# Optimization experiments

Measured on AMD Instinct MI355X. Metric: run time of the kernel, lower is better.

## Reference

```python
import jax, jax.numpy as jnp
import numpy as np

NUM_NODES = 100000
NUM_REL = 3
IN_C, HID_C, OUT_C = 128, 64, 32
E, P = 1600000, 200000


def setup_inputs() -> dict:
    key = jax.random.key(0)
    ks = jax.random.split(key, 16)
    inp = {
        "x": jax.random.normal(ks[0], (NUM_NODES, IN_C), dtype=jnp.float32),
        "edge_index": jax.random.randint(ks[1], (2, E), 0, NUM_NODES),
        "edge_type": jax.random.randint(ks[2], (E,), 0, NUM_REL),
        "pred_edges": jax.random.randint(ks[3], (2, P), 0, NUM_NODES),
        # RGCN layer 1
        "W1": jax.random.normal(ks[4], (NUM_REL, IN_C, HID_C), dtype=jnp.float32) * 0.05,
        "root1": jax.random.normal(ks[5], (IN_C, HID_C), dtype=jnp.float32) * 0.05,
        "b1": jnp.zeros((HID_C,), dtype=jnp.float32),
        # RGCN layer 2
        "W2": jax.random.normal(ks[6], (NUM_REL, HID_C, OUT_C), dtype=jnp.float32) * 0.05,
        "root2": jax.random.normal(ks[7], (HID_C, OUT_C), dtype=jnp.float32) * 0.05,
        "b2": jnp.zeros((OUT_C,), dtype=jnp.float32),
        # decoder MLP: Linear(2*OUT_C, HID_C) -> ReLU -> Linear(HID_C, 1)
        "Wd1": jax.random.normal(ks[8], (2 * OUT_C, HID_C), dtype=jnp.float32) * 0.05,
        "bd1": jnp.zeros((HID_C,), dtype=jnp.float32),
        "Wd2": jax.random.normal(ks[9], (HID_C, 1), dtype=jnp.float32) * 0.05,
        "bd2": jnp.zeros((1,), dtype=jnp.float32),
    }
    return inp


def rgcn_conv(x, edge_index, edge_type, W, root, b):
    """PyG RGCNConv: per-relation mean aggregation + root transform + bias."""
    src, dst = edge_index[0], edge_index[1]
    n = x.shape[0]
    xs = x[src]  # [E, in] single gather reused across relations
    out = x @ root + b
    for r in range(W.shape[0]):  # small fixed relation count
        mask = (edge_type == r)
        msg = jnp.where(mask[:, None], xs @ W[r], 0.0)  # [E, out]
        summed = jax.ops.segment_sum(msg, dst, num_segments=n)
        cnt = jax.ops.segment_sum(mask.astype(x.dtype), dst, num_segments=n)
        out = out + summed / jnp.maximum(cnt, 1.0)[:, None]
    return out


def reference(x, edge_index, edge_type, pred_edges, W1, root1, b1, W2, root2, b2, Wd1, bd1, Wd2, bd2):
    # encode (eval mode: dropout is identity)
    z = jax.nn.relu(rgcn_conv(x, edge_index, edge_type, W1, root1, b1))
    z = rgcn_conv(z, edge_index, edge_type, W2, root2, b2)
    # decode
    src, dst = pred_edges[0], pred_edges[1]
    ef = jnp.concatenate([z[src], z[dst]], axis=1)  # [P, 2*OUT_C]
    h = jax.nn.relu(ef @ Wd1 + bd1)
    return (h @ Wd2 + bd2).squeeze(-1)  # [P]
```

## Files before the change

### kernel.cpp

```cpp
#include <hip/hip_runtime.h>
#include <hip/hip_bf16.h>


typedef short bf16x8 __attribute__((ext_vector_type(8)));
typedef float f32x4 __attribute__((ext_vector_type(4)));
typedef float f32x2 __attribute__((ext_vector_type(2)));

__device__ __forceinline__ unsigned short f2bf(float f) {
  union { float f; unsigned u; } x; x.f = f;
  unsigned r = x.u + 0x7FFF + ((x.u >> 16) & 1);
  return (unsigned short)(r >> 16);
}
__device__ __forceinline__ float bf2f(unsigned short h) {
  union { unsigned u; float f; } x; x.u = ((unsigned)h) << 16;
  return x.f;
}
__device__ __forceinline__ f32x2 bfpair(unsigned u) {
  union { unsigned u; float f; } a, b;
  a.u = u << 16; b.u = u & 0xFFFF0000u;
  f32x2 r; r[0] = a.f; r[1] = b.f; return r;
}
__device__ __forceinline__ unsigned pk2(float a, float b) {
  return (unsigned)f2bf(a) | ((unsigned)f2bf(b) << 16);
}

template <int K, int TN>
__device__ __forceinline__ void pack_one(
    int e, const float* __restrict__ W, const float* __restrict__ root,
    ushort* __restrict__ Bh, ushort* __restrict__ Bl) {
  int slab = e / (K * TN), r = e % (K * TN);
  int k = r / TN, n = r % TN;
  float v = (slab < 3) ? W[(size_t)slab * K * TN + k * TN + n] : root[(size_t)k * TN + n];
  int kc = k >> 5, quad = (k >> 3) & 3, j = k & 7, nt = n >> 4, nn = n & 15;
  int NTt = TN / 16;
  int didx = slab * K * TN + ((kc * NTt + nt) * 64 + quad * 16 + nn) * 8 + j;
  unsigned short h = f2bf(v);
  Bh[didx] = h;
  Bl[didx] = f2bf(v - bf2f(h));
}

__global__ __launch_bounds__(256) void hist_pack_kernel(
    const int* __restrict__ ei, int* __restrict__ hist, int E, int tile, int NBUCK,
    const float* __restrict__ W1, const float* __restrict__ root1,
    ushort* __restrict__ Bh1, ushort* __restrict__ Bl1,
    const float* __restrict__ W2, const float* __restrict__ root2,
    ushort* __restrict__ Bh2, ushort* __restrict__ Bl2) {
  int tid = threadIdx.x;
  if (blockIdx.x >= 256) {
    int e = (blockIdx.x - 256) * 256 + tid;
    if (e < 32768) pack_one<128, 64>(e, W1, root1, Bh1, Bl1);
    else if (e < 32768 + 8192) pack_one<64, 32>(e - 32768, W2, root2, Bh2, Bl2);
    return;
  }
  __shared__ int lh[512];
  for (int i = tid; i < 512; i += 256) lh[i] = 0;
  __syncthreads();
  int e0 = blockIdx.x * tile, e1 = min(E, e0 + tile);
  for (int e = e0 + tid; e < e1; e += 256) atomicAdd(&lh[ei[E + e] >> 8], 1);
  __syncthreads();
  for (int i = tid; i < NBUCK; i += 256) hist[i * 256 + blockIdx.x] = lh[i];
}

__global__ __launch_bounds__(256) void scan_rows_kernel(
    int* __restrict__ hist, int* __restrict__ rowsum) {
  __shared__ int sA[256], sB[256];
  int t = threadIdx.x;
  int* row = hist + blockIdx.x * 256;
  int v = row[t];
  sA[t] = v;
  __syncthreads();
  int* src = sA; int* dst = sB;
  for (int off = 1; off < 256; off <<= 1) {
    int x = src[t];
    if (t >= off) x += src[t - off];
    dst[t] = x;
    __syncthreads();
    int* tmp = src; src = dst; dst = tmp;
  }
  row[t] = src[t] - v;
  if (t == 255) rowsum[blockIdx.x] = src[255];
}

__global__ __launch_bounds__(512) void scan_top_kernel(
    const int* __restrict__ rowsum, int* __restrict__ rowbase, int NBUCK, int E) {
  __shared__ int sA[512], sB[512];
  int t = threadIdx.x;
  int v = (t < NBUCK) ? rowsum[t] : 0;
  sA[t] = v;
  __syncthreads();
  int* src = sA; int* dst = sB;
  for (int off = 1; off < 512; off <<= 1) {
    int x = src[t];
    if (t >= off) x += src[t - off];
    dst[t] = x;
    __syncthreads();
    int* tmp = src; src = dst; dst = tmp;
  }
  if (t < NBUCK) rowbase[t] = src[t] - v;
  if (t == 0) rowbase[NBUCK] = E;
}

__global__ __launch_bounds__(256) void part_scatter_kernel(
    const int* __restrict__ ei, const int* __restrict__ et,
    const int* __restrict__ hist, const int* __restrict__ rowbase,
    unsigned* __restrict__ rec, int E, int tile, int NBUCK) {
  __shared__ int ctr[512];
  int tid = threadIdx.x;
  for (int i = tid; i < NBUCK; i += 256)
    ctr[i] = hist[i * 256 + blockIdx.x] + rowbase[i];
  __syncthreads();
  int e0 = blockIdx.x * tile, e1 = min(E, e0 + tile);
  for (int e = e0 + tid; e < e1; e += 256) {
    int s = ei[e];
    int d = ei[E + e];
    int t = et[e];
    int p = atomicAdd(&ctr[d >> 8], 1);
    rec[p] = (unsigned)(s | (t << 20) | ((d & 255) << 22));
  }
}

__global__ __launch_bounds__(256) void bucket_build_kernel(
    const unsigned* __restrict__ rec, const int* __restrict__ rowbase,
    float4* __restrict__ inv4, int2* __restrict__ sd,
    int* __restrict__ eSrcT, int N) {
  __shared__ int c3[768];
  __shared__ int sA[256], sB[256];
  __shared__ int cur[256];
  int tid = threadIdx.x;
  int dstBase = blockIdx.x << 8;
  int bs = rowbase[blockIdx.x], be = rowbase[blockIdx.x + 1];
  for (int i = tid; i < 768; i += 256) c3[i] = 0;
  __syncthreads();
  for (int i = bs + tid; i < be; i += 256) {
    unsigned r = rec[i];
    atomicAdd(&c3[((r >> 20) & 3) * 256 + (r >> 22)], 1);
  }
  __syncthreads();
  int c0 = c3[tid], c1 = c3[256 + tid], c2 = c3[512 + tid];
  int dgv = c0 + c1 + c2;
  sA[tid] = dgv;
  if (dstBase + tid < N) {
    inv4[dstBase + tid] = make_float4(1.0f / (float)max(c0, 1),
                                      1.0f / (float)max(c1, 1),
                                      1.0f / (float)max(c2, 1), 0.f);
  }
  __syncthreads();
  int* src = sA; int* dst = sB;
  for (int off = 1; off < 256; off <<= 1) {
    int x = src[tid];
    if (tid >= off) x += src[tid - off];
    dst[tid] = x;
    __syncthreads();
    int* tmp = src; src = dst; dst = tmp;
  }
  int excl = src[tid] - dgv;
  cur[tid] = bs + excl;
  if (dstBase + tid < N) sd[dstBase + tid] = make_int2(bs + excl, dgv);
  __syncthreads();
  for (int i = bs + tid; i < be; i += 256) {
    unsigned r = rec[i];
    int p = atomicAdd(&cur[r >> 22], 1);
    eSrcT[p] = (int)(r & 0x3FFFFF);
  }
}

template <int K, int TN>
__global__ __launch_bounds__(256, 4) void mfma_gemm_kernel(
    const float* __restrict__ A, const ushort* __restrict__ Bh,
    const ushort* __restrict__ Bl, const float* __restrict__ bias,
    ushort* __restrict__ Hb, float* __restrict__ z, int n) {
  constexpr int KC = K / 32;
  constexpr int NTt = TN / 16;
  constexpr int HALF = K * TN / 8;
  __shared__ int4 bsm[2 * HALF];
  const int tid = threadIdx.x;
  const int w = tid >> 6, lane = tid & 63;
  const int quad = lane >> 4, nn = lane & 15;
  const int rowBase = blockIdx.x * 64 + w * 16;

  int row = rowBase + nn;
  if (row >= n) row = n - 1;
  const float* ap = &A[(size_t)row * K + quad * 8];
  bf16x8 ah[KC], al[KC];
#pragma unroll
  for (int kc = 0; kc < KC; kc++) {
    float4 f0 = *(const float4*)(ap + kc * 32);
    float4 f1 = *(const float4*)(ap + kc * 32 + 4);
    float f[8] = {f0.x, f0.y, f0.z, f0.w, f1.x, f1.y, f1.z, f1.w};
#pragma unroll
    for (int j = 0; j < 8; j++) {
      unsigned short h = f2bf(f[j]);
      ah[kc][j] = (short)h;
      al[kc][j] = (short)f2bf(f[j] - bf2f(h));
    }
  }

  const short* bsp = (const short*)bsm;

#pragma unroll 1
  for (int slab = 0; slab < 4; slab++) {
    __syncthreads();
    {
      const int4* gh = (const int4*)(Bh + (size_t)slab * K * TN);
      for (int i = tid; i < HALF; i += 256) bsm[i] = gh[i];
      if (slab == 3) {
        const int4* gl = (const int4*)(Bl + (size_t)slab * K * TN);
        for (int i = tid; i < HALF; i += 256) bsm[HALF + i] = gl[i];
      }
    }
    __syncthreads();

    f32x4 acc[NTt];
#pragma unroll
    for (int j = 0; j < NTt; j++) acc[j] = (f32x4){0.f, 0.f, 0.f, 0.f};

#pragma unroll
    for (int kc = 0; kc < KC; kc++) {
#pragma unroll
      for (int nt = 0; nt < NTt; nt++) {
        bf16x8 b = *(const bf16x8*)&bsp[((kc * NTt + nt) * 64 + lane) * 8];
        acc[nt] = __builtin_amdgcn_mfma_f32_16x16x32_bf16(ah[kc], b, acc[nt], 0, 0, 0);
        acc[nt] = __builtin_amdgcn_mfma_f32_16x16x32_bf16(al[kc], b, acc[nt], 0, 0, 0);
      }
    }
    if (slab == 3) {
#pragma unroll
      for (int kc = 0; kc < KC; kc++) {
#pragma unroll
        for (int nt = 0; nt < NTt; nt++) {
          bf16x8 b = *(const bf16x8*)&bsp[(HALF * 8) + ((kc * NTt + nt) * 64 + lane) * 8];
          acc[nt] = __builtin_amdgcn_mfma_f32_16x16x32_bf16(ah[kc], b, acc[nt], 0, 0, 0);
        }
      }
    }

    int grow0 = rowBase + quad * 4;
#pragma unroll
    for (int nt = 0; nt < NTt; nt++) {
      int col = nt * 16 + nn;
#pragma unroll
      for (int rg = 0; rg < 4; rg++) {
        int grow = grow0 + rg;
        if (grow < n) {
          float v = acc[nt][rg];
          if (slab == 3) z[(size_t)grow * TN + col] = v + bias[col];
          else Hb[((size_t)slab * n + grow) * TN + col] = f2bf(v);
        }
      }
    }
  }
}

__global__ __launch_bounds__(256, 4) void mfma_gemm2_kernel(
    const ushort* __restrict__ Ab, const ushort* __restrict__ Bh,
    const ushort* __restrict__ Bl, const float* __restrict__ bias,
    ushort* __restrict__ Hb, float* __restrict__ z2r, int n) {
  constexpr int KC = 2, NTt = 2, HALF = 64 * 32 / 8;
  __shared__ int4 bsm[2 * HALF];
  const int tid = threadIdx.x;
  const int w = tid >> 6, lane = tid & 63;
  const int quad = lane >> 4, nn = lane & 15;
  const int rowBase = blockIdx.x * 64 + w * 16;

  int row = rowBase + nn;
  if (row >= n) row = n - 1;
  const ushort* ap = &Ab[(size_t)row * 64 + quad * 8];
  bf16x8 ah[KC];
  ah[0] = *(const bf16x8*)(ap);
  ah[1] = *(const bf16x8*)(ap + 32);

  const short* bsp = (const short*)bsm;

#pragma unroll 1
  for (int slab = 0; slab < 4; slab++) {
    __syncthreads();
    {
      const int4* gh = (const int4*)(Bh + (size_t)slab * 64 * 32);
      for (int i = tid; i < HALF; i += 256) bsm[i] = gh[i];
      if (slab == 3) {
        const int4* gl = (const int4*)(Bl + (size_t)slab * 64 * 32);
        for (int i = tid; i < HALF; i += 256) bsm[HALF + i] = gl[i];
      }
    }
    __syncthreads();

    f32x4 acc[NTt];
#pragma unroll
    for (int j = 0; j < NTt; j++) acc[j] = (f32x4){0.f, 0.f, 0.f, 0.f};

#pragma unroll
    for (int kc = 0; kc < KC; kc++) {
#pragma unroll
      for (int nt = 0; nt < NTt; nt++) {
        bf16x8 b = *(const bf16x8*)&bsp[((kc * NTt + nt) * 64 + lane) * 8];
        acc[nt] = __builtin_amdgcn_mfma_f32_16x16x32_bf16(ah[kc], b, acc[nt], 0, 0, 0);
      }
    }
    if (slab == 3) {
#pragma unroll
      for (int kc = 0; kc < KC; kc++) {
#pragma unroll
        for (int nt = 0; nt < NTt; nt++) {
          bf16x8 b = *(const bf16x8*)&bsp[(HALF * 8) + ((kc * NTt + nt) * 64 + lane) * 8];
          acc[nt] = __builtin_amdgcn_mfma_f32_16x16x32_bf16(ah[kc], b, acc[nt], 0, 0, 0);
        }
      }
    }

    int grow0 = rowBase + quad * 4;
#pragma unroll
    for (int nt = 0; nt < NTt; nt++) {
      int col = nt * 16 + nn;
#pragma unroll
      for (int rg = 0; rg < 4; rg++) {
        int grow = grow0 + rg;
        if (grow < n) {
          float v = acc[nt][rg];
          if (slab == 3) z2r[(size_t)grow * 32 + col] = v + bias[col];
          else Hb[((size_t)slab * n + grow) * 32 + col] = f2bf(v);
        }
      }
    }
  }
}

__global__ __launch_bounds__(256) void pull64_kernel(
    const ushort* __restrict__ Hb, const int* __restrict__ eSrcT,
    const int2* __restrict__ sd, const float4* __restrict__ inv4,
    const float* __restrict__ z1r, ushort* __restrict__ z1b, int N) {
  int w = (blockIdx.x * 256 + threadIdx.x) >> 6;
  if (w >= N) return;
  int lane = threadIdx.x & 63;
  int g = lane >> 3, q = lane & 7;
  int2 s2 = sd[w];
  float4 iv = inv4[w];
  f32x2 acc0 = {0.f, 0.f}, acc1 = acc0, acc2 = acc0, acc3 = acc0;
  for (int i = g; i < s2.y; i += 8) {
    int p = eSrcT[s2.x + i];
    int s = p & 0xFFFFF, t = p >> 20;
    float sc = (t == 0) ? iv.x : ((t == 1) ? iv.y : iv.z);
    f32x2 sc2 = {sc, sc};
    uint4 v = *(const uint4*)&Hb[((size_t)t * N + s) * 64 + q * 8];
    acc0 += bfpair(v.x) * sc2;
    acc1 += bfpair(v.y) * sc2;
    acc2 += bfpair(v.z) * sc2;
    acc3 += bfpair(v.w) * sc2;
  }
  float a[8] = {acc0[0], acc0[1], acc1[0], acc1[1], acc2[0], acc2[1], acc3[0], acc3[1]};
#pragma unroll
  for (int m = 8; m <= 32; m <<= 1)
#pragma unroll
    for (int j = 0; j < 8; j++) a[j] += __shfl_xor(a[j], m);
  if (g == 0) {
    const float4* zr = (const float4*)&z1r[(size_t)w * 64 + q * 8];
    float4 r0 = zr[0], r1 = zr[1];
    float o0 = fmaxf(r0.x + a[0], 0.f), o1 = fmaxf(r0.y + a[1], 0.f);
    float o2 = fmaxf(r0.z + a[2], 0.f), o3 = fmaxf(r0.w + a[3], 0.f);
    float o4 = fmaxf(r1.x + a[4], 0.f), o5 = fmaxf(r1.y + a[5], 0.f);
    float o6 = fmaxf(r1.z + a[6], 0.f), o7 = fmaxf(r1.w + a[7], 0.f);
    uint4 st;
    st.x = pk2(o0, o1); st.y = pk2(o2, o3); st.z = pk2(o4, o5); st.w = pk2(o6, o7);
    *(uint4*)&z1b[(size_t)w * 64 + q * 8] = st;
  }
}

__global__ __launch_bounds__(256) void pull32_kernel(
    const ushort* __restrict__ Hb, const int* __restrict__ eSrcT,
    const int2* __restrict__ sd, const float4* __restrict__ inv4,
    const float* __restrict__ z2r, ushort* __restrict__ z2b, int N) {
  int w = (blockIdx.x * 256 + threadIdx.x) >> 6;
  if (w >= N) return;
  int lane = threadIdx.x & 63;
  int g = lane >> 2, q = lane & 3;
  int2 s2 = sd[w];
  float4 iv = inv4[w];
  f32x2 acc0 = {0.f, 0.f}, acc1 = acc0, acc2 = acc0, acc3 = acc0;
  for (int i = g; i < s2.y; i += 16) {
    int p = eSrcT[s2.x + i];
    int s = p & 0xFFFFF, t = p >> 20;
    float sc = (t == 0) ? iv.x : ((t == 1) ? iv.y : iv.z);
    f32x2 sc2 = {sc, sc};
    uint4 v = *(const uint4*)&Hb[((size_t)t * N + s) * 32 + q * 8];
    acc0 += bfpair(v.x) * sc2;
    acc1 += bfpair(v.y) * sc2;
    acc2 += bfpair(v.z) * sc2;
    acc3 += bfpair(v.w) * sc2;
  }
  float a[8] = {acc0[0], acc0[1], acc1[0], acc1[1], acc2[0], acc2[1], acc3[0], acc3[1]};
#pragma unroll
  for (int m = 4; m <= 32; m <<= 1)
#pragma unroll
    for (int j = 0; j < 8; j++) a[j] += __shfl_xor(a[j], m);
  if (g == 0) {
    const float4* zr = (const float4*)&z2r[(size_t)w * 32 + q * 8];
    float4 r0 = zr[0], r1 = zr[1];
    uint4 st;
    st.x = pk2(r0.x + a[0], r0.y + a[1]);
    st.y = pk2(r0.z + a[2], r0.w + a[3]);
    st.z = pk2(r1.x + a[4], r1.y + a[5]);
    st.w = pk2(r1.z + a[6], r1.w + a[7]);
    *(uint4*)&z2b[(size_t)w * 32 + q * 8] = st;
  }
}

__global__ __launch_bounds__(256) void decoder_kernel(
    const ushort* __restrict__ z2b, const int* __restrict__ pe,
    const float* __restrict__ Wd1, const float* __restrict__ bd1,
    const float* __restrict__ Wd2, const float* __restrict__ bd2,
    float* __restrict__ out, int P) {
  __shared__ float W[64 * 64];
  __shared__ float w2[64], b1s[64];
  int tid = threadIdx.x;
  for (int i = tid * 4; i < 4096; i += 1024) *(float4*)&W[i] = *(const float4*)&Wd1[i];
  if (tid < 64) {
    w2[tid] = Wd2[tid];
    b1s[tid] = bd1[tid];
  }
  __syncthreads();
  int p = blockIdx.x * 256 + tid;
  if (p >= P) return;
  int s = pe[p];
  int d = pe[P + p];
  float zs[32], zd[32];
  const uint4* ps4 = (const uint4*)&z2b[(size_t)s * 32];
  const uint4* pd4 = (const uint4*)&z2b[(size_t)d * 32];
#pragma unroll
  for (int i = 0; i < 4; i++) {
    uint4 u = ps4[i];
    f32x2 p0 = bfpair(u.x), p1 = bfpair(u.y), p2 = bfpair(u.z), p3 = bfpair(u.w);
    zs[8 * i + 0] = p0[0]; zs[8 * i + 1] = p0[1];
    zs[8 * i + 2] = p1[0]; zs[8 * i + 3] = p1[1];
    zs[8 * i + 4] = p2[0]; zs[8 * i + 5] = p2[1];
    zs[8 * i + 6] = p3[0]; zs[8 * i + 7] = p3[1];
    uint4 v = pd4[i];
    f32x2 q0 = bfpair(v.x), q1 = bfpair(v.y), q2 = bfpair(v.z), q3 = bfpair(v.w);
    zd[8 * i + 0] = q0[0]; zd[8 * i + 1] = q0[1];
    zd[8 * i + 2] = q1[0]; zd[8 * i + 3] = q1[1];
    zd[8 * i + 4] = q2[0]; zd[8 * i + 5] = q2[1];
    zd[8 * i + 6] = q3[0]; zd[8 * i + 7] = q3[1];
  }
  float acc = bd2[0];
#pragma unroll 4
  for (int j = 0; j < 64; j++) {
    float h = b1s[j];
#pragma unroll
    for (int i = 0; i < 32; i++) h += zs[i] * W[i * 64 + j];
#pragma unroll
    for (int i = 0; i < 32; i++) h += zd[i] * W[(32 + i) * 64 + j];
    h = fmaxf(h, 0.0f);
    acc += h * w2[j];
  }
  out[p] = acc;
}

extern "C" void kernel_launch(void* const* d_in, const int* in_sizes, int n_in,
                              void* d_out, int out_size, void* d_ws, size_t ws_size,
                              hipStream_t stream) {
  const float* x     = (const float*)d_in[0];
  const int*   ei    = (const int*)d_in[1];
  const int*   et    = (const int*)d_in[2];
  const int*   pe    = (const int*)d_in[3];
  const float* W1    = (const float*)d_in[4];
  const float* root1 = (const float*)d_in[5];
  const float* b1    = (const float*)d_in[6];
  const float* W2    = (const float*)d_in[7];
  const float* root2 = (const float*)d_in[8];
  const float* b2    = (const float*)d_in[9];
  const float* Wd1   = (const float*)d_in[10];
  const float* bd1   = (const float*)d_in[11];
  const float* Wd2   = (const float*)d_in[12];
  const float* bd2   = (const float*)d_in[13];
  float* out = (float*)d_out;

  const int N = in_sizes[0] / 128;
  const int E = in_sizes[2];
  const int P = in_sizes[3] / 2;

  const int NBUCK = (N + 255) >> 8;
  const int tile  = (E + 255) / 256;

  float* ws   = (float*)d_ws;
  float4* inv4 = (float4*)ws;
  float* z1r  = ws + (size_t)4 * N;
  ushort* z1b = (ushort*)(ws + (size_t)68 * N);
  float* z2r  = ws + (size_t)100 * N;
  ushort* z2b = (ushort*)(ws + (size_t)132 * N);
  ushort* Hb  = (ushort*)(ws + (size_t)148 * N);
  ushort* Bh1 = (ushort*)(ws + (size_t)244 * N);
  ushort* Bl1 = Bh1 + 32768;
  ushort* Bh2 = Bl1 + 32768;
  ushort* Bl2 = Bh2 + 8192;
  int* ib      = (int*)(ws + (size_t)245 * N);
  int2* sd     = (int2*)ib;
  int* rowbase = ib + 2 * (size_t)N;
  int* rowsum  = rowbase + 1024;
  int* hist    = rowsum + 1024;
  size_t roff = 2 * (size_t)N + 2048 + (size_t)NBUCK * 256;
  roff = (roff + 3) & ~(size_t)3;
  unsigned* rec = (unsigned*)(ib + roff);
  int* eSrcT  = ib + roff + (size_t)E;

  hist_pack_kernel<<<256 + 160, 256, 0, stream>>>(
      ei, hist, E, tile, NBUCK, W1, root1, Bh1, Bl1, W2, root2, Bh2, Bl2);
  scan_rows_kernel<<<NBUCK, 256, 0, stream>>>(hist, rowsum);
  scan_top_kernel<<<1, 512, 0, stream>>>(rowsum, rowbase, NBUCK, E);
  part_scatter_kernel<<<256, 256, 0, stream>>>(ei, et, hist, rowbase, rec, E, tile, NBUCK);
  bucket_build_kernel<<<NBUCK, 256, 0, stream>>>(rec, rowbase, inv4, sd, eSrcT, N);

  const int gb = (N + 63) / 64;
  const int pullBlocks = (N * 64 + 255) / 256;

  mfma_gemm_kernel<128, 64><<<gb, 256, 0, stream>>>(x, Bh1, Bl1, b1, Hb, z1r, N);
  pull64_kernel<<<pullBlocks, 256, 0, stream>>>(Hb, eSrcT, sd, inv4, z1r, z1b, N);

  mfma_gemm2_kernel<<<gb, 256, 0, stream>>>(z1b, Bh2, Bl2, b2, Hb, z2r, N);
  pull32_kernel<<<pullBlocks, 256, 0, stream>>>(Hb, eSrcT, sd, inv4, z2r, z2b, N);

  decoder_kernel<<<(P + 255) / 256, 256, 0, stream>>>(z2b, pe, Wd1, bd1, Wd2, bd2, out, P);
}
```

Before: 342.1 us.

## Precompute per-edge scales, shrink pull kernels to lane groups, MFMA decoder

The bucket build now writes per-edge records that hold the pre-offset Hb row index and the inverse degree scale, so the inv4 array goes away. The pull kernels drop from one wavefront per node to 8 or 4 lanes per node, which removes the cross-lane shuffle reductions. The decoder MLP first layer now runs on bf16 MFMA with a pre-packed Wd1 tile instead of scalar FP32 FMAs. In exchange, edge records double in size, each node's edges are walked serially by fewer lanes, and the decoder loses some precision by rounding Wd1 to bf16.

```diff
diff --git a/kernel.cpp b/kernel.cpp
--- a/kernel.cpp
+++ b/kernel.cpp
@@ -44,12 +44,21 @@
     const float* __restrict__ W1, const float* __restrict__ root1,
     ushort* __restrict__ Bh1, ushort* __restrict__ Bl1,
     const float* __restrict__ W2, const float* __restrict__ root2,
-    ushort* __restrict__ Bh2, ushort* __restrict__ Bl2) {
+    ushort* __restrict__ Bh2, ushort* __restrict__ Bl2,
+    const float* __restrict__ Wd1, ushort* __restrict__ Bd1h) {
   int tid = threadIdx.x;
   if (blockIdx.x >= 256) {
     int e = (blockIdx.x - 256) * 256 + tid;
-    if (e < 32768) pack_one<128, 64>(e, W1, root1, Bh1, Bl1);
-    else if (e < 32768 + 8192) pack_one<64, 32>(e - 32768, W2, root2, Bh2, Bl2);
+    if (e < 32768) {
+      pack_one<128, 64>(e, W1, root1, Bh1, Bl1);
+    } else if (e < 32768 + 8192) {
+      pack_one<64, 32>(e - 32768, W2, root2, Bh2, Bl2);
+    } else if (e < 32768 + 8192 + 4096) {
+      int r = e - 32768 - 8192;
+      int k = r >> 6, n = r & 63;
+      int kc = k >> 5, quad = (k >> 3) & 3, j = k & 7, nt = n >> 4, nn = n & 15;
+      Bd1h[((kc * 4 + nt) * 64 + quad * 16 + nn) * 8 + j] = f2bf(Wd1[k * 64 + n]);
+    }
     return;
   }
   __shared__ int lh[512];
@@ -121,8 +130,7 @@
 
 __global__ __launch_bounds__(256) void bucket_build_kernel(
     const unsigned* __restrict__ rec, const int* __restrict__ rowbase,
-    float4* __restrict__ inv4, int2* __restrict__ sd,
-    int* __restrict__ eSrcT, int N) {
+    int2* __restrict__ sd, int2* __restrict__ erec, int N) {
   __shared__ int c3[768];
   __shared__ int sA[256], sB[256];
   __shared__ int cur[256];
@@ -136,14 +144,8 @@
     atomicAdd(&c3[((r >> 20) & 3) * 256 + (r >> 22)], 1);
   }
   __syncthreads();
-  int c0 = c3[tid], c1 = c3[256 + tid], c2 = c3[512 + tid];
-  int dgv = c0 + c1 + c2;
+  int dgv = c3[tid] + c3[256 + tid] + c3[512 + tid];
   sA[tid] = dgv;
-  if (dstBase + tid < N) {
-    inv4[dstBase + tid] = make_float4(1.0f / (float)max(c0, 1),
-                                      1.0f / (float)max(c1, 1),
-                                      1.0f / (float)max(c2, 1), 0.f);
-  }
   __syncthreads();
   int* src = sA; int* dst = sB;
   for (int off = 1; off < 256; off <<= 1) {
@@ -159,8 +161,11 @@
   __syncthreads();
   for (int i = bs + tid; i < be; i += 256) {
     unsigned r = rec[i];
-    int p = atomicAdd(&cur[r >> 22], 1);
-    eSrcT[p] = (int)(r & 0x3FFFFF);
+    int dloc = r >> 22;
+    int t = (r >> 20) & 3;
+    int p = atomicAdd(&cur[dloc], 1);
+    float sc = 1.0f / (float)max(c3[t * 256 + dloc], 1);
+    erec[p] = make_int2(t * N + (int)(r & 0xFFFFF), __float_as_int(sc));
   }
 }
 
@@ -325,132 +330,119 @@
 }
 
 __global__ __launch_bounds__(256) void pull64_kernel(
-    const ushort* __restrict__ Hb, const int* __restrict__ eSrcT,
-    const int2* __restrict__ sd, const float4* __restrict__ inv4,
-    const float* __restrict__ z1r, ushort* __restrict__ z1b, int N) {
-  int w = (blockIdx.x * 256 + threadIdx.x) >> 6;
+    const ushort* __restrict__ Hb, const int2* __restrict__ erec,
+    const int2* __restrict__ sd, const float* __restrict__ z1r,
+    ushort* __restrict__ z1b, int N) {
+  int w = (blockIdx.x * 256 + threadIdx.x) >> 3;
   if (w >= N) return;
-  int lane = threadIdx.x & 63;
-  int g = lane >> 3, q = lane & 7;
+  int q = threadIdx.x & 7;
   int2 s2 = sd[w];
-  float4 iv = inv4[w];
-  f32x2 acc0 = {0.f, 0.f}, acc1 = acc0, acc2 = acc0, acc3 = acc0;
-  for (int i = g; i < s2.y; i += 8) {
-    int p = eSrcT[s2.x + i];
-    int s = p & 0xFFFFF, t = p >> 20;
-    float sc = (t == 0) ? iv.x : ((t == 1) ? iv.y : iv.z);
+  f32x2 a0 = {0.f, 0.f}, a1 = a0, a2 = a0, a3 = a0;
+  for (int i = 0; i < s2.y; i++) {
+    int2 r = erec[s2.x + i];
+    float sc = __int_as_float(r.y);
     f32x2 sc2 = {sc, sc};
-    uint4 v = *(const uint4*)&Hb[((size_t)t * N + s) * 64 + q * 8];
-    acc0 += bfpair(v.x) * sc2;
-    acc1 += bfpair(v.y) * sc2;
-    acc2 += bfpair(v.z) * sc2;
-    acc3 += bfpair(v.w) * sc2;
-  }
-  float a[8] = {acc0[0], acc0[1], acc1[0], acc1[1], acc2[0], acc2[1], acc3[0], acc3[1]};
-#pragma unroll
-  for (int m = 8; m <= 32; m <<= 1)
-#pragma unroll
-    for (int j = 0; j < 8; j++) a[j] += __shfl_xor(a[j], m);
-  if (g == 0) {
-    const float4* zr = (const float4*)&z1r[(size_t)w * 64 + q * 8];
-    float4 r0 = zr[0], r1 = zr[1];
-    float o0 = fmaxf(r0.x + a[0], 0.f), o1 = fmaxf(r0.y + a[1], 0.f);
-    float o2 = fmaxf(r0.z + a[2], 0.f), o3 = fmaxf(r0.w + a[3], 0.f);
-    float o4 = fmaxf(r1.x + a[4], 0.f), o5 = fmaxf(r1.y + a[5], 0.f);
-    float o6 = fmaxf(r1.z + a[6], 0.f), o7 = fmaxf(r1.w + a[7], 0.f);
-    uint4 st;
-    st.x = pk2(o0, o1); st.y = pk2(o2, o3); st.z = pk2(o4, o5); st.w = pk2(o6, o7);
-    *(uint4*)&z1b[(size_t)w * 64 + q * 8] = st;
-  }
+    uint4 v = *(const uint4*)&Hb[(size_t)r.x * 64 + q * 8];
+    a0 += bfpair(v.x) * sc2;
+    a1 += bfpair(v.y) * sc2;
+    a2 += bfpair(v.z) * sc2;
+    a3 += bfpair(v.w) * sc2;
+  }
+  const float4* zr = (const float4*)&z1r[(size_t)w * 64 + q * 8];
+  float4 r0 = zr[0], r1 = zr[1];
+  uint4 st;
+  st.x = pk2(fmaxf(r0.x + a0[0], 0.f), fmaxf(r0.y + a0[1], 0.f));
+  st.y = pk2(fmaxf(r0.z + a1[0], 0.f), fmaxf(r0.w + a1[1], 0.f));
+  st.z = pk2(fmaxf(r1.x + a2[0], 0.f), fmaxf(r1.y + a2[1], 0.f));
+  st.w = pk2(fmaxf(r1.z + a3[0], 0.f), fmaxf(r1.w + a3[1], 0.f));
+  *(uint4*)&z1b[(size_t)w * 64 + q * 8] = st;
 }
 
 __global__ __launch_bounds__(256) void pull32_kernel(
-    const ushort* __restrict__ Hb, const int* __restrict__ eSrcT,
-    const int2* __restrict__ sd, const float4* __restrict__ inv4,
-    const float* __restrict__ z2r, ushort* __restrict__ z2b, int N) {
-  int w = (blockIdx.x * 256 + threadIdx.x) >> 6;
+    const ushort* __restrict__ Hb, const int2* __restrict__ erec,
+    const int2* __restrict__ sd, const float* __restrict__ z2r,
+    ushort* __restrict__ z2b, int N) {
+  int w = (blockIdx.x * 256 + threadIdx.x) >> 2;
   if (w >= N) return;
-  int lane = threadIdx.x & 63;
-  int g = lane >> 2, q = lane & 3;
+  int q = threadIdx.x & 3;
   int2 s2 = sd[w];
-  float4 iv = inv4[w];
-  f32x2 acc0 = {0.f, 0.f}, acc1 = acc0, acc2 = acc0, acc3 = acc0;
-  for (int i = g; i < s2.y; i += 16) {
-    int p = eSrcT[s2.x + i];
-    int s = p & 0xFFFFF, t = p >> 20;
-    float sc = (t == 0) ? iv.x : ((t == 1) ? iv.y : iv.z);
+  f32x2 a0 = {0.f, 0.f}, a1 = a0, a2 = a0, a3 = a0;
+  for (int i = 0; i < s2.y; i++) {
+    int2 r = erec[s2.x + i];
+    float sc = __int_as_float(r.y);
     f32x2 sc2 = {sc, sc};
-    uint4 v = *(const uint4*)&Hb[((size_t)t * N + s) * 32 + q * 8];
-    acc0 += bfpair(v.x) * sc2;
-    acc1 += bfpair(v.y) * sc2;
-    acc2 += bfpair(v.z) * sc2;
-    acc3 += bfpair(v.w) * sc2;
-  }
-  float a[8] = {acc0[0], acc0[1], acc1[0], acc1[1], acc2[0], acc2[1], acc3[0], acc3[1]};
-#pragma unroll
-  for (int m = 4; m <= 32; m <<= 1)
-#pragma unroll
-    for (int j = 0; j < 8; j++) a[j] += __shfl_xor(a[j], m);
-  if (g == 0) {
-    const float4* zr = (const float4*)&z2r[(size_t)w * 32 + q * 8];
-    float4 r0 = zr[0], r1 = zr[1];
-    uint4 st;
-    st.x = pk2(r0.x + a[0], r0.y + a[1]);
-    st.y = pk2(r0.z + a[2], r0.w + a[3]);
-    st.z = pk2(r1.x + a[4], r1.y + a[5]);
-    st.w = pk2(r1.z + a[6], r1.w + a[7]);
-    *(uint4*)&z2b[(size_t)w * 32 + q * 8] = st;
-  }
+    uint4 v = *(const uint4*)&Hb[(size_t)r.x * 32 + q * 8];
+    a0 += bfpair(v.x) * sc2;
+    a1 += bfpair(v.y) * sc2;
+    a2 += bfpair(v.z) * sc2;
+    a3 += bfpair(v.w) * sc2;
+  }
+  const float4* zr = (const float4*)&z2r[(size_t)w * 32 + q * 8];
+  float4 r0 = zr[0], r1 = zr[1];
+  uint4 st;
+  st.x = pk2(r0.x + a0[0], r0.y + a0[1]);
+  st.y = pk2(r0.z + a1[0], r0.w + a1[1]);
+  st.z = pk2(r1.x + a2[0], r1.y + a2[1]);
+  st.w = pk2(r1.z + a3[0], r1.w + a3[1]);
+  *(uint4*)&z2b[(size_t)w * 32 + q * 8] = st;
 }
 
 __global__ __launch_bounds__(256) void decoder_kernel(
     const ushort* __restrict__ z2b, const int* __restrict__ pe,
-    const float* __restrict__ Wd1, const float* __restrict__ bd1,
+    const ushort* __restrict__ Bd1h, const float* __restrict__ bd1,
     const float* __restrict__ Wd2, const float* __restrict__ bd2,
     float* __restrict__ out, int P) {
-  __shared__ float W[64 * 64];
-  __shared__ float w2[64], b1s[64];
+  __shared__ int4 wsm[512];
+  __shared__ float b1s[64], w2s[64];
   int tid = threadIdx.x;
-  for (int i = tid * 4; i < 4096; i += 1024) *(float4*)&W[i] = *(const float4*)&Wd1[i];
-  if (tid < 64) {
-    w2[tid] = Wd2[tid];
-    b1s[tid] = bd1[tid];
-  }
-  __syncthreads();
-  int p = blockIdx.x * 256 + tid;
-  if (p >= P) return;
-  int s = pe[p];
-  int d = pe[P + p];
-  float zs[32], zd[32];
-  const uint4* ps4 = (const uint4*)&z2b[(size_t)s * 32];
-  const uint4* pd4 = (const uint4*)&z2b[(size_t)d * 32];
-#pragma unroll
-  for (int i = 0; i < 4; i++) {
-    uint4 u = ps4[i];
-    f32x2 p0 = bfpair(u.x), p1 = bfpair(u.y), p2 = bfpair(u.z), p3 = bfpair(u.w);
-    zs[8 * i + 0] = p0[0]; zs[8 * i + 1] = p0[1];
-    zs[8 * i + 2] = p1[0]; zs[8 * i + 3] = p1[1];
-    zs[8 * i + 4] = p2[0]; zs[8 * i + 5] = p2[1];
-    zs[8 * i + 6] = p3[0]; zs[8 * i + 7] = p3[1];
-    uint4 v = pd4[i];
-    f32x2 q0 = bfpair(v.x), q1 = bfpair(v.y), q2 = bfpair(v.z), q3 = bfpair(v.w);
-    zd[8 * i + 0] = q0[0]; zd[8 * i + 1] = q0[1];
-    zd[8 * i + 2] = q1[0]; zd[8 * i + 3] = q1[1];
-    zd[8 * i + 4] = q2[0]; zd[8 * i + 5] = q2[1];
-    zd[8 * i + 6] = q3[0]; zd[8 * i + 7] = q3[1];
-  }
-  float acc = bd2[0];
-#pragma unroll 4
-  for (int j = 0; j < 64; j++) {
-    float h = b1s[j];
-#pragma unroll
-    for (int i = 0; i < 32; i++) h += zs[i] * W[i * 64 + j];
-#pragma unroll
-    for (int i = 0; i < 32; i++) h += zd[i] * W[(32 + i) * 64 + j];
-    h = fmaxf(h, 0.0f);
-    acc += h * w2[j];
-  }
-  out[p] = acc;
+  {
+    const int4* g = (const int4*)Bd1h;
+    for (int i = tid; i < 512; i += 256) wsm[i] = g[i];
+    if (tid < 64) { b1s[tid] = bd1[tid]; w2s[tid] = Wd2[tid]; }
+  }
+  __syncthreads();
+  const short* bsp = (const short*)wsm;
+  int wv = tid >> 6, lane = tid & 63;
+  int quad = lane >> 4, nn = lane & 15;
+  int p0 = blockIdx.x * 64 + wv * 16;
+  int p = min(p0 + nn, P - 1);
+  int s = pe[p], d = pe[P + p];
+  bf16x8 a0 = *(const bf16x8*)&z2b[(size_t)s * 32 + quad * 8];
+  bf16x8 a1 = *(const bf16x8*)&z2b[(size_t)d * 32 + quad * 8];
+  f32x4 acc[4];
+#pragma unroll
+  for (int nt = 0; nt < 4; nt++) acc[nt] = (f32x4){0.f, 0.f, 0.f, 0.f};
+#pragma unroll
+  for (int nt = 0; nt < 4; nt++) {
+    bf16x8 b0 = *(const bf16x8*)&bsp[((0 * 4 + nt) * 64 + lane) * 8];
+    acc[nt] = __builtin_amdgcn_mfma_f32_16x16x32_bf16(a0, b0, acc[nt], 0, 0, 0);
+    bf16x8 b1 = *(const bf16x8*)&bsp[((1 * 4 + nt) * 64 + lane) * 8];
+    acc[nt] = __builtin_amdgcn_mfma_f32_16x16x32_bf16(a1, b1, acc[nt], 0, 0, 0);
+  }
+  float part[4];
+#pragma unroll
+  for (int rg = 0; rg < 4; rg++) {
+    float t = 0.f;
+#pragma unroll
+    for (int nt = 0; nt < 4; nt++) {
+      int col = nt * 16 + nn;
+      float h = fmaxf(acc[nt][rg] + b1s[col], 0.f);
+      t += h * w2s[col];
+    }
+    part[rg] = t;
+  }
+#pragma unroll
+  for (int m = 1; m <= 8; m <<= 1)
+#pragma unroll
+    for (int rg = 0; rg < 4; rg++) part[rg] += __shfl_xor(part[rg], m);
+  if (nn == 0) {
+    float base = bd2[0];
+#pragma unroll
+    for (int rg = 0; rg < 4; rg++) {
+      int po = p0 + quad * 4 + rg;
+      if (po < P) out[po] = part[rg] + base;
+    }
+  }
 }
 
 extern "C" void kernel_launch(void* const* d_in, const int* in_sizes, int n_in,
@@ -480,41 +472,39 @@
   const int tile  = (E + 255) / 256;
 
   float* ws   = (float*)d_ws;
-  float4* inv4 = (float4*)ws;
-  float* z1r  = ws + (size_t)4 * N;
-  ushort* z1b = (ushort*)(ws + (size_t)68 * N);
-  float* z2r  = ws + (size_t)100 * N;
-  ushort* z2b = (ushort*)(ws + (size_t)132 * N);
-  ushort* Hb  = (ushort*)(ws + (size_t)148 * N);
-  ushort* Bh1 = (ushort*)(ws + (size_t)244 * N);
+  float* z1r  = ws;
+  ushort* z1b = (ushort*)(ws + (size_t)64 * N);
+  float* z2r  = ws + (size_t)96 * N;
+  ushort* z2b = (ushort*)(ws + (size_t)128 * N);
+  ushort* Hb  = (ushort*)(ws + (size_t)144 * N);
+  ushort* Bh1 = (ushort*)(ws + (size_t)240 * N);
   ushort* Bl1 = Bh1 + 32768;
   ushort* Bh2 = Bl1 + 32768;
   ushort* Bl2 = Bh2 + 8192;
-  int* ib      = (int*)(ws + (size_t)245 * N);
+  ushort* Bd1h = Bl2 + 8192;
+  int* ib      = (int*)(ws + (size_t)241 * N);
   int2* sd     = (int2*)ib;
-  int* rowbase = ib + 2 * (size_t)N;
+  int2* erec   = (int2*)(ib + 2 * (size_t)N);
+  int* rowbase = ib + 2 * (size_t)N + 2 * (size_t)E;
   int* rowsum  = rowbase + 1024;
   int* hist    = rowsum + 1024;
-  size_t roff = 2 * (size_t)N + 2048 + (size_t)NBUCK * 256;
-  roff = (roff + 3) & ~(size_t)3;
-  unsigned* rec = (unsigned*)(ib + roff);
-  int* eSrcT  = ib + roff + (size_t)E;
-
-  hist_pack_kernel<<<256 + 160, 256, 0, stream>>>(
-      ei, hist, E, tile, NBUCK, W1, root1, Bh1, Bl1, W2, root2, Bh2, Bl2);
+  unsigned* rec = (unsigned*)(hist + (size_t)NBUCK * 256);
+
+  hist_pack_kernel<<<256 + 176, 256, 0, stream>>>(
+      ei, hist, E, tile, NBUCK, W1, root1, Bh1, Bl1, W2, root2, Bh2, Bl2,
+      Wd1, Bd1h);
   scan_rows_kernel<<<NBUCK, 256, 0, stream>>>(hist, rowsum);
   scan_top_kernel<<<1, 512, 0, stream>>>(rowsum, rowbase, NBUCK, E);
   part_scatter_kernel<<<256, 256, 0, stream>>>(ei, et, hist, rowbase, rec, E, tile, NBUCK);
-  bucket_build_kernel<<<NBUCK, 256, 0, stream>>>(rec, rowbase, inv4, sd, eSrcT, N);
+  bucket_build_kernel<<<NBUCK, 256, 0, stream>>>(rec, rowbase, sd, erec, N);
 
   const int gb = (N + 63) / 64;
-  const int pullBlocks = (N * 64 + 255) / 256;
 
   mfma_gemm_kernel<128, 64><<<gb, 256, 0, stream>>>(x, Bh1, Bl1, b1, Hb, z1r, N);
-  pull64_kernel<<<pullBlocks, 256, 0, stream>>>(Hb, eSrcT, sd, inv4, z1r, z1b, N);
+  pull64_kernel<<<((size_t)N * 8 + 255) / 256, 256, 0, stream>>>(Hb, erec, sd, z1r, z1b, N);
 
   mfma_gemm2_kernel<<<gb, 256, 0, stream>>>(z1b, Bh2, Bl2, b2, Hb, z2r, N);
-  pull32_kernel<<<pullBlocks, 256, 0, stream>>>(Hb, eSrcT, sd, inv4, z2r, z2b, N);
-
-  decoder_kernel<<<(P + 255) / 256, 256, 0, stream>>>(z2b, pe, Wd1, bd1, Wd2, bd2, out, P);
-}
+  pull32_kernel<<<((size_t)N * 4 + 255) / 256, 256, 0, stream>>>(Hb, erec, sd, z2r, z2b, N);
+
+  decoder_kernel<<<(P + 63) / 64, 256, 0, stream>>>(z2b, pe, Bd1h, bd1, Wd2, bd2, out, P);
+}
```

New measurement: 305.5 us. 1.12x faster.
